# Kernel optimization log

Hardware: AMD Instinct MI355X
Metric: run time of the kernel (lower is better)

Reference implementation:

```python
import jax, jax.numpy as jnp
import numpy as np

DIM = 256
HEADS = 4
HEAD_DIM = DIM // HEADS
SCALE = HEAD_DIM ** -0.5


def setup_inputs() -> dict:
    key = jax.random.key(0)
    ks = jax.random.split(key, 6)
    B, N, C = 4, 4096, DIM
    x = jax.random.normal(ks[0], (B, N, C), dtype=jnp.float32)
    # torch.nn.Linear weights are [out, in]; y = x @ W.T (+ b)
    s = 1.0 / np.sqrt(C)
    Wq = jax.random.uniform(ks[1], (C, C), jnp.float32, -s, s)
    Wk = jax.random.uniform(ks[2], (C, C), jnp.float32, -s, s)
    Wv = jax.random.uniform(ks[3], (C, C), jnp.float32, -s, s)
    Wp = jax.random.uniform(ks[4], (C, C), jnp.float32, -s, s)
    bp = jax.random.uniform(ks[5], (C,), jnp.float32, -s, s)
    return {"x": x, "Wq": Wq, "Wk": Wk, "Wv": Wv, "Wp": Wp, "bp": bp}


def reference(x, Wq, Wk, Wv, Wp, bp):
    B, N, C = x.shape
    H, D = HEADS, HEAD_DIM
    # project and split heads: [B, H, N, D]
    def heads(W):
        return (x @ W.T).reshape(B, N, H, D).transpose(0, 2, 1, 3)
    q = heads(Wq)
    k = heads(Wk)
    v = heads(Wv)
    attn = jnp.einsum('bhnd,bhmd->bhnm', q, k) * SCALE  # [B,H,N,N]
    attn = jax.nn.softmax(attn, axis=-1)
    out = jnp.einsum('bhnm,bhmd->bhnd', attn, v)  # [B,H,N,D]
    out = out.transpose(0, 2, 1, 3).reshape(B, N, C)
    return out @ Wp.T + bp
```

## Files before the change

### kernel.cpp

```cpp
#include <hip/hip_runtime.h>

typedef unsigned short u16t;
typedef unsigned int u32t;
typedef __bf16 bf16x8 __attribute__((ext_vector_type(8)));
typedef float f32x4 __attribute__((ext_vector_type(4)));
typedef float f32x16 __attribute__((ext_vector_type(16)));
typedef unsigned int u32x4 __attribute__((ext_vector_type(4)));
typedef unsigned int u32x2 __attribute__((ext_vector_type(2)));

#define DEV static __device__ __forceinline__

DEV u16t f2bf(float f){
  u32t u = __builtin_bit_cast(u32t, f);
  u += 0x7fffu + ((u >> 16) & 1u);
  return (u16t)(u >> 16);
}

DEV u32t cvtpk(float lo, float hi){
  u32t r;
  asm("v_cvt_pk_bf16_f32 %0, %1, %2" : "=v"(r) : "v"(lo), "v"(hi));
  return r;
}

DEV void plswap(u32t &a, u32t &b){
  asm("v_permlane32_swap_b32 %0, %1" : "+v"(a), "+v"(b));
}

DEV float fexp2(float x){
#if __has_builtin(__builtin_amdgcn_exp2f)
  return __builtin_amdgcn_exp2f(x);
#else
  return exp2f(x);
#endif
}

DEV void gll16(const void* g, void* l){
  __builtin_amdgcn_global_load_lds((const __attribute__((address_space(1))) void*)g,
                                   (__attribute__((address_space(3))) void*)l, 16, 0, 0);
}

DEV f32x4 mfma16(bf16x8 a, bf16x8 b, f32x4 c){
  return __builtin_amdgcn_mfma_f32_16x16x32_bf16(a, b, c, 0, 0, 0);
}

DEV f32x16 mfma32(bf16x8 a, bf16x8 b, f32x16 c){
  return __builtin_amdgcn_mfma_f32_32x32x16_bf16(a, b, c, 0, 0, 0);
}

__global__ __launch_bounds__(256) void k_cast_x(const float4* __restrict__ x, u16t* __restrict__ xb){
  int idx = blockIdx.x * 256 + threadIdx.x;
  float4 v = x[idx];
  ushort4 o = make_ushort4(f2bf(v.x), f2bf(v.y), f2bf(v.z), f2bf(v.w));
  *(ushort4*)&xb[idx * 4] = o;
}

__global__ __launch_bounds__(256) void k_cast_w(const float* __restrict__ Wq, const float* __restrict__ Wk,
                         const float* __restrict__ Wv, const float* __restrict__ Wp,
                         u16t* __restrict__ wqkv, u16t* __restrict__ wp){
  int idx = blockIdx.x * 256 + threadIdx.x;
  if (idx < 196608){
    float v;
    if (idx < 65536)        v = Wq[idx] * 0.1803368801f;
    else if (idx < 131072)  v = Wk[idx - 65536];
    else                    v = Wv[idx - 131072];
    wqkv[idx] = f2bf(v);
  } else {
    int j = idx - 196608;
    wp[j] = f2bf(Wp[j]);
  }
}

template<bool IS_QKV>
__global__ __launch_bounds__(256) void k_gemm(const u16t* __restrict__ A, const u16t* __restrict__ W,
    const float* __restrict__ bias, u16t* __restrict__ oq, u16t* __restrict__ okk, u16t* __restrict__ vtg,
    float* __restrict__ op, int Ntot){
  __shared__ u32x4 sm[1536];
  const int tid = threadIdx.x, lane = tid & 63, w = tid >> 6, g = lane >> 4, li = lane & 15;
  const int m0 = blockIdx.x * 128, n0 = blockIdx.y * 64;
  const int wm = w >> 1, wn = w & 1;
  f32x4 acc[4][2] = {};
  for (int kk = 0; kk < 4; ++kk){
    #pragma unroll
    for (int rnd = 0; rnd < 4; ++rnd){
      int cid = rnd * 256 + tid;
      int row = cid >> 3, ch = cid & 7;
      const u16t* src = A + (m0 + row) * 256 + kk * 64 + ((ch ^ (row & 7)) << 3);
      gll16(src, (char*)sm + (rnd * 256 + w * 64) * 16);
    }
    #pragma unroll
    for (int rnd = 0; rnd < 2; ++rnd){
      int cid = rnd * 256 + tid;
      int row = cid >> 3, ch = cid & 7;
      const u16t* src = W + (n0 + row) * 256 + kk * 64 + ((ch ^ (row & 7)) << 3);
      gll16(src, (char*)sm + 16384 + (rnd * 256 + w * 64) * 16);
    }
    __syncthreads();
    #pragma unroll
    for (int ks = 0; ks < 2; ++ks){
      bf16x8 bfr[2];
      #pragma unroll
      for (int nj = 0; nj < 2; ++nj){
        int row = wn * 32 + nj * 16 + li;
        bfr[nj] = __builtin_bit_cast(bf16x8, sm[1024 + row * 8 + ((ks * 4 + g) ^ (row & 7))]);
      }
      #pragma unroll
      for (int mi = 0; mi < 4; ++mi){
        int row = wm * 64 + mi * 16 + li;
        bf16x8 af = __builtin_bit_cast(bf16x8, sm[row * 8 + ((ks * 4 + g) ^ (row & 7))]);
        #pragma unroll
        for (int nj = 0; nj < 2; ++nj)
          acc[mi][nj] = mfma16(af, bfr[nj], acc[mi][nj]);
      }
    }
    __syncthreads();
  }
  if (IS_QKV){
    const int which = n0 >> 8, h = (n0 >> 6) & 3;
    if (which == 2){
      u16t* smv = (u16t*)sm;
      #pragma unroll
      for (int mi = 0; mi < 4; ++mi){
        #pragma unroll
        for (int nj = 0; nj < 2; ++nj){
          int d = wn * 32 + nj * 16 + li;
          int mloc = wm * 64 + mi * 16 + g * 4;
          u32x2 pk2;
          pk2.x = cvtpk(acc[mi][nj][0], acc[mi][nj][1]);
          pk2.y = cvtpk(acc[mi][nj][2], acc[mi][nj][3]);
          int chk = mloc >> 3, inner = (mloc & 7) * 2;
          *(u32x2*)((char*)smv + d * 256 + (((chk ^ (d & 7))) << 4) + inner) = pk2;
        }
      }
      __syncthreads();
      const int b = m0 >> 12, bh2 = b * 4 + h, mbase = m0 & 4095;
      #pragma unroll
      for (int rnd = 0; rnd < 4; ++rnd){
        int qq = rnd * 256 + tid;
        int d = qq & 63, cidx = qq >> 6;
        u32x4 val = *(const u32x4*)((char*)smv + d * 256 + ((cidx ^ (d & 7)) << 4));
        int nt = (mbase >> 6) + (cidx >> 3), i = cidx & 7;
        *(u32x4*)((char*)vtg + ((((size_t)bh2 * 64 + nt) * 8 + i) * 64 + d) * 16) = val;
      }
    } else if (which == 1){
      #pragma unroll
      for (int mi = 0; mi < 4; ++mi){
        int m = m0 + wm * 64 + mi * 16 + g * 4;
        int b = m >> 12;
        #pragma unroll
        for (int nj = 0; nj < 2; ++nj){
          int d = wn * 32 + nj * 16 + li;
          int kk2 = d >> 4, dhi = (d >> 3) & 1, e = d & 7;
          #pragma unroll
          for (int r = 0; r < 4; ++r){
            int row = (m + r) & 4095;
            int nt = row >> 6, jt = (row >> 5) & 1, pp = row & 31;
            okk[(size_t)(b * 4 + h) * 262144 + nt * 4096 + (kk2 * 2 + jt) * 512 + dhi * 256 + pp * 8 + e]
              = f2bf(acc[mi][nj][r]);
          }
        }
      }
    } else {
      #pragma unroll
      for (int mi = 0; mi < 4; ++mi){
        int m = m0 + wm * 64 + mi * 16 + g * 4;
        int b = m >> 12, nn = m & 4095;
        #pragma unroll
        for (int nj = 0; nj < 2; ++nj){
          int d = wn * 32 + nj * 16 + li;
          #pragma unroll
          for (int r = 0; r < 4; ++r)
            oq[((b * 4 + h) * 4096 + nn + r) * 64 + d] = f2bf(acc[mi][nj][r]);
        }
      }
    }
  } else {
    #pragma unroll
    for (int mi = 0; mi < 4; ++mi){
      int m = m0 + wm * 64 + mi * 16 + g * 4;
      #pragma unroll
      for (int nj = 0; nj < 2; ++nj){
        int n = n0 + wn * 32 + nj * 16 + li;
        float bv = bias[n];
        #pragma unroll
        for (int r = 0; r < 4; ++r)
          op[(m + r) * Ntot + n] = acc[mi][nj][r] + bv;
      }
    }
  }
}

__global__ __launch_bounds__(512) void k_flash(const u16t* __restrict__ q,
    const u16t* __restrict__ kslot, const u16t* __restrict__ vslot, u16t* __restrict__ ao){
  __shared__ char sm[66560];
  const int tid = threadIdx.x, lane = tid & 63, w = tid >> 6;
  const int hi = lane >> 5, p = lane & 31;
  const int kvh = w >> 2, qg = w & 3;
  const int bid = blockIdx.x;
  const int swz = (bid & 7) * 64 + (bid >> 3);
  const int bh = swz >> 5, qt = swz & 31;
  const int rowbase = qt * 128 + qg * 32;
  const int r256 = tid & 255;
  const char* kbB = (const char*)kslot + (size_t)bh * 524288 + (size_t)kvh * 262144 + r256 * 16;
  const char* vbB = (const char*)vslot + (size_t)bh * 524288 + (size_t)kvh * 262144 + r256 * 16;
  char* myLds = sm + kvh * 32768;

  auto stage = [&](int t, int c){
    char* dst = myLds + c * 16384 + r256 * 16;
    const char* sK = kbB + (size_t)t * 8192;
    const char* sV = vbB + (size_t)t * 8192;
    gll16(sK, dst);
    gll16(sK + 4096, dst + 4096);
    gll16(sV, dst + 8192);
    gll16(sV + 4096, dst + 12288);
  };

  u32x4 qf[4];
  #pragma unroll
  for (int kk = 0; kk < 4; ++kk)
    qf[kk] = *(const u32x4*)&q[((size_t)bh * 4096 + rowbase + p) * 64 + kk * 16 + hi * 8];
  asm volatile("s_waitcnt vmcnt(0)" ::: "memory");
  stage(0, 0);
  stage(1, 1);

  f32x16 ot[2] = {};
  float lsp[4] = {};
  const f32x16 fz = {};

  #pragma unroll 1
  for (int t = 0; t < 32; ++t){
    asm volatile("s_waitcnt vmcnt(4)" ::: "memory");
    __builtin_amdgcn_s_barrier();
    asm volatile("" ::: "memory");
    const char* Kb = myLds + (t & 1) * 16384;
    const char* Vt = Kb + 8192;
    f32x16 st[2];
    #pragma unroll
    for (int kk = 0; kk < 4; ++kk)
      #pragma unroll
      for (int jt = 0; jt < 2; ++jt){
        bf16x8 kf = __builtin_bit_cast(bf16x8,
            *(const u32x4*)(Kb + (kk * 2 + jt) * 1024 + lane * 16));
        st[jt] = mfma32(kf, __builtin_bit_cast(bf16x8, qf[kk]), kk == 0 ? fz : st[jt]);
      }
    #pragma unroll
    for (int jt = 0; jt < 2; ++jt){
      float e[16];
      #pragma unroll
      for (int r = 0; r < 16; ++r)
        e[r] = fexp2(st[jt][r]);
      #pragma unroll
      for (int r = 0; r < 16; ++r)
        lsp[r & 3] += e[r];
      u32x4 pf[2];
      #pragma unroll
      for (int s = 0; s < 2; ++s){
        u32t a0 = cvtpk(e[s*8+0], e[s*8+1]);
        u32t a1 = cvtpk(e[s*8+2], e[s*8+3]);
        u32t b0 = cvtpk(e[s*8+4], e[s*8+5]);
        u32t b1 = cvtpk(e[s*8+6], e[s*8+7]);
        plswap(a0, b0);
        plswap(a1, b1);
        pf[s] = (u32x4){a0, a1, b0, b1};
      }
      #pragma unroll
      for (int s = 0; s < 2; ++s)
        #pragma unroll
        for (int dt = 0; dt < 2; ++dt){
          bf16x8 vf = __builtin_bit_cast(bf16x8,
              *(const u32x4*)(Vt + ((jt * 2 + s) * 2 + hi) * 1024 + dt * 512 + p * 16));
          ot[dt] = mfma32(vf, __builtin_bit_cast(bf16x8, pf[s]), ot[dt]);
        }
    }
    asm volatile("s_waitcnt lgkmcnt(0)" ::: "memory");
    __builtin_amdgcn_s_barrier();
    asm volatile("" ::: "memory");
    stage((t + 2) & 31, t & 1);
  }
  asm volatile("s_waitcnt vmcnt(0)" ::: "memory");
  __builtin_amdgcn_s_barrier();
  asm volatile("" ::: "memory");

  float l = (lsp[0] + lsp[1]) + (lsp[2] + lsp[3]);
  l += __shfl_xor(l, 32);
  float* lsums = (float*)(sm + 65536);
  if (lane < 32) lsums[w * 32 + lane] = l;

  {
    char* reg = sm + w * 8192;
    #pragma unroll
    for (int dt = 0; dt < 2; ++dt)
      #pragma unroll
      for (int s4 = 0; s4 < 4; ++s4){
        f32x4 v4 = {ot[dt][4*s4+0], ot[dt][4*s4+1], ot[dt][4*s4+2], ot[dt][4*s4+3]};
        int quad = 2 * s4 + hi + 8 * dt;
        *(f32x4*)(reg + p * 256 + ((quad ^ (p & 15)) << 4)) = v4;
      }
  }
  __syncthreads();

  {
    const int qrow = tid >> 2, seg = tid & 3;
    const int qg2 = qrow >> 5, qloc = qrow & 31;
    float ltot = lsums[qg2 * 32 + qloc] + lsums[(4 + qg2) * 32 + qloc];
    float inv = __builtin_amdgcn_rcpf(ltot);
    const int b = bh >> 2, head = bh & 3;
    u32t pko[8];
    #pragma unroll
    for (int k = 0; k < 4; ++k){
      int quad = seg * 4 + k;
      int off = qloc * 256 + ((quad ^ (qloc & 15)) << 4);
      f32x4 s = *(const f32x4*)(sm + qg2 * 8192 + off)
              + *(const f32x4*)(sm + (4 + qg2) * 8192 + off);
      s = s * inv;
      pko[2*k]   = cvtpk(s[0], s[1]);
      pko[2*k+1] = cvtpk(s[2], s[3]);
    }
    u16t* dst = ao + ((size_t)b * 4096 + qt * 128 + qrow) * 256 + head * 64 + seg * 16;
    *(u32x4*)(dst)     = (u32x4){pko[0], pko[1], pko[2], pko[3]};
    *(u32x4*)(dst + 8) = (u32x4){pko[4], pko[5], pko[6], pko[7]};
  }
}

extern "C" void kernel_launch(void* const* d_in, const int* in_sizes, int n_in,
                              void* d_out, int out_size, void* d_ws, size_t ws_size,
                              hipStream_t stream){
  (void)in_sizes; (void)n_in; (void)out_size; (void)ws_size;
  const float* x  = (const float*)d_in[0];
  const float* Wq = (const float*)d_in[1];
  const float* Wk = (const float*)d_in[2];
  const float* Wv = (const float*)d_in[3];
  const float* Wp = (const float*)d_in[4];
  const float* bp = (const float*)d_in[5];
  float* out = (float*)d_out;

  u16t* ws   = (u16t*)d_ws;
  u16t* xb   = ws;
  u16t* qg   = ws + 4194304;
  u16t* kg   = ws + 8388608;
  u16t* vtg  = ws + 12582912;
  u16t* ao   = ws + 16777216;
  u16t* wqkv = ws + 20971520;
  u16t* wpb  = ws + 21168128;

  k_cast_x<<<4096, 256, 0, stream>>>((const float4*)x, xb);
  k_cast_w<<<1024, 256, 0, stream>>>(Wq, Wk, Wv, Wp, wqkv, wpb);
  k_gemm<true><<<dim3(128, 12), 256, 0, stream>>>(xb, wqkv, nullptr, qg, kg, vtg, nullptr, 768);
  k_flash<<<512, 512, 0, stream>>>(qg, kg, vtg, ao);
  k_gemm<false><<<dim3(128, 4), 256, 0, stream>>>(ao, wpb, bp, nullptr, nullptr, nullptr, out, 256);
}
```

Measured before the change: 107.5 us.

## Halve flash block size and load K fragments directly into registers

```diff
diff --git a/kernel.cpp b/kernel.cpp
--- a/kernel.cpp
+++ b/kernel.cpp
@@ -189,59 +189,70 @@
   }
 }
 
-__global__ __launch_bounds__(512) void k_flash(const u16t* __restrict__ q,
+__global__ __launch_bounds__(256) void k_flash(const u16t* __restrict__ q,
     const u16t* __restrict__ kslot, const u16t* __restrict__ vslot, u16t* __restrict__ ao){
-  __shared__ char sm[66560];
+  __shared__ char sm[33280];
   const int tid = threadIdx.x, lane = tid & 63, w = tid >> 6;
   const int hi = lane >> 5, p = lane & 31;
-  const int kvh = w >> 2, qg = w & 3;
+  const int kvh = w >> 1, qg = w & 1;
   const int bid = blockIdx.x;
-  const int swz = (bid & 7) * 64 + (bid >> 3);
-  const int bh = swz >> 5, qt = swz & 31;
-  const int rowbase = qt * 128 + qg * 32;
-  const int r256 = tid & 255;
-  const char* kbB = (const char*)kslot + (size_t)bh * 524288 + (size_t)kvh * 262144 + r256 * 16;
-  const char* vbB = (const char*)vslot + (size_t)bh * 524288 + (size_t)kvh * 262144 + r256 * 16;
-  char* myLds = sm + kvh * 32768;
-
-  auto stage = [&](int t, int c){
-    char* dst = myLds + c * 16384 + r256 * 16;
-    const char* sK = kbB + (size_t)t * 8192;
-    const char* sV = vbB + (size_t)t * 8192;
-    gll16(sK, dst);
-    gll16(sK + 4096, dst + 4096);
-    gll16(sV, dst + 8192);
-    gll16(sV + 4096, dst + 12288);
+  const int swz = (bid & 7) * 128 + (bid >> 3);
+  const int bh = swz >> 6, qt = swz & 63;
+  const int rowbase = qt * 64 + qg * 32;
+  const int r128 = tid & 127;
+  const char* kbB = (const char*)kslot + (size_t)bh * 524288 + (size_t)kvh * 262144 + lane * 16;
+  const char* vbB = (const char*)vslot + (size_t)bh * 524288 + (size_t)kvh * 262144 + r128 * 16;
+  char* Vbuf = sm + kvh * 16384;
+
+  auto stageV = [&](int t, int c){
+    char* dst = Vbuf + c * 8192 + r128 * 16;
+    const char* s = vbB + (size_t)t * 8192;
+    gll16(s,        dst);
+    gll16(s + 2048, dst + 2048);
+    gll16(s + 4096, dst + 4096);
+    gll16(s + 6144, dst + 6144);
   };
 
   u32x4 qf[4];
   #pragma unroll
   for (int kk = 0; kk < 4; ++kk)
     qf[kk] = *(const u32x4*)&q[((size_t)bh * 4096 + rowbase + p) * 64 + kk * 16 + hi * 8];
-  asm volatile("s_waitcnt vmcnt(0)" ::: "memory");
-  stage(0, 0);
-  stage(1, 1);
 
   f32x16 ot[2] = {};
   float lsp[4] = {};
+  u32x4 kreg[2][4];
   const f32x16 fz = {};
+
+  #pragma unroll
+  for (int jt = 0; jt < 2; ++jt)
+    #pragma unroll
+    for (int kk = 0; kk < 4; ++kk)
+      kreg[jt][kk] = *(const u32x4*)(kbB + (kk * 2 + jt) * 1024);
+  stageV(0, 0);
+  stageV(1, 1);
 
   #pragma unroll 1
   for (int t = 0; t < 32; ++t){
-    asm volatile("s_waitcnt vmcnt(4)" ::: "memory");
+    asm volatile("s_waitcnt vmcnt(0)" ::: "memory");
     __builtin_amdgcn_s_barrier();
     asm volatile("" ::: "memory");
-    const char* Kb = myLds + (t & 1) * 16384;
-    const char* Vt = Kb + 8192;
     f32x16 st[2];
     #pragma unroll
     for (int kk = 0; kk < 4; ++kk)
       #pragma unroll
       for (int jt = 0; jt < 2; ++jt){
-        bf16x8 kf = __builtin_bit_cast(bf16x8,
-            *(const u32x4*)(Kb + (kk * 2 + jt) * 1024 + lane * 16));
+        bf16x8 kf = __builtin_bit_cast(bf16x8, kreg[jt][kk]);
         st[jt] = mfma32(kf, __builtin_bit_cast(bf16x8, qf[kk]), kk == 0 ? fz : st[jt]);
       }
+    {
+      const char* kb = kbB + (size_t)((t + 1) & 31) * 8192;
+      #pragma unroll
+      for (int jt = 0; jt < 2; ++jt)
+        #pragma unroll
+        for (int kk = 0; kk < 4; ++kk)
+          kreg[jt][kk] = *(const u32x4*)(kb + (kk * 2 + jt) * 1024);
+    }
+    const char* Vt = Vbuf + (t & 1) * 8192;
     #pragma unroll
     for (int jt = 0; jt < 2; ++jt){
       float e[16];
@@ -267,22 +278,21 @@
         #pragma unroll
         for (int dt = 0; dt < 2; ++dt){
           bf16x8 vf = __builtin_bit_cast(bf16x8,
-              *(const u32x4*)(Vt + ((jt * 2 + s) * 2 + hi) * 1024 + dt * 512 + p * 16));
+              *(const u32x4*)(Vt + (jt * 2 + s) * 2048 + hi * 1024 + dt * 512 + p * 16));
           ot[dt] = mfma32(vf, __builtin_bit_cast(bf16x8, pf[s]), ot[dt]);
         }
     }
     asm volatile("s_waitcnt lgkmcnt(0)" ::: "memory");
     __builtin_amdgcn_s_barrier();
     asm volatile("" ::: "memory");
-    stage((t + 2) & 31, t & 1);
+    stageV((t + 2) & 31, t & 1);
   }
   asm volatile("s_waitcnt vmcnt(0)" ::: "memory");
-  __builtin_amdgcn_s_barrier();
-  asm volatile("" ::: "memory");
+  __syncthreads();
 
   float l = (lsp[0] + lsp[1]) + (lsp[2] + lsp[3]);
   l += __shfl_xor(l, 32);
-  float* lsums = (float*)(sm + 65536);
+  float* lsums = (float*)(sm + 32768);
   if (lane < 32) lsums[w * 32 + lane] = l;
 
   {
@@ -301,7 +311,7 @@
   {
     const int qrow = tid >> 2, seg = tid & 3;
     const int qg2 = qrow >> 5, qloc = qrow & 31;
-    float ltot = lsums[qg2 * 32 + qloc] + lsums[(4 + qg2) * 32 + qloc];
+    float ltot = lsums[qg2 * 32 + qloc] + lsums[(2 + qg2) * 32 + qloc];
     float inv = __builtin_amdgcn_rcpf(ltot);
     const int b = bh >> 2, head = bh & 3;
     u32t pko[8];
@@ -310,12 +320,12 @@
       int quad = seg * 4 + k;
       int off = qloc * 256 + ((quad ^ (qloc & 15)) << 4);
       f32x4 s = *(const f32x4*)(sm + qg2 * 8192 + off)
-              + *(const f32x4*)(sm + (4 + qg2) * 8192 + off);
+              + *(const f32x4*)(sm + (2 + qg2) * 8192 + off);
       s = s * inv;
       pko[2*k]   = cvtpk(s[0], s[1]);
       pko[2*k+1] = cvtpk(s[2], s[3]);
     }
-    u16t* dst = ao + ((size_t)b * 4096 + qt * 128 + qrow) * 256 + head * 64 + seg * 16;
+    u16t* dst = ao + ((size_t)b * 4096 + qt * 64 + qrow) * 256 + head * 64 + seg * 16;
     *(u32x4*)(dst)     = (u32x4){pko[0], pko[1], pko[2], pko[3]};
     *(u32x4*)(dst + 8) = (u32x4){pko[4], pko[5], pko[6], pko[7]};
   }
@@ -345,6 +355,6 @@
   k_cast_x<<<4096, 256, 0, stream>>>((const float4*)x, xb);
   k_cast_w<<<1024, 256, 0, stream>>>(Wq, Wk, Wv, Wp, wqkv, wpb);
   k_gemm<true><<<dim3(128, 12), 256, 0, stream>>>(xb, wqkv, nullptr, qg, kg, vtg, nullptr, 768);
-  k_flash<<<512, 512, 0, stream>>>(qg, kg, vtg, ao);
+  k_flash<<<1024, 256, 0, stream>>>(qg, kg, vtg, ao);
   k_gemm<false><<<dim3(128, 4), 256, 0, stream>>>(ao, wpb, bp, nullptr, nullptr, nullptr, out, 256);
 }
```

After: 116.6 us. 1.08x slower.
